# Performance work log

Hardware: AMD Instinct MI355X
Metric: run time of the kernel (lower is better)

## Reference

```python
import jax, jax.numpy as jnp
import numpy as np

V, E, H, S, B = 32000, 512, 512, 512, 32  # vocab, emb=n_unit, hidden, srclen, batch


def _lstm_zero_state_step(x, W_ih, b_ih, b_hh):
    """PyTorch LSTM single step with zero initial (h, c).
    With h0 = 0, the recurrent term h0 @ W_hh^T vanishes, so W_hh does not
    affect the output (faithful to the original, which never passes state).
    Gate order i, f, g, o. Works on [..., in_dim] batched inputs.
    """
    gates = x @ W_ih.T + b_ih + b_hh
    i, f, g, o = jnp.split(gates, 4, axis=-1)
    c = jax.nn.sigmoid(i) * jnp.tanh(g)  # f gate multiplies c0 = 0
    h = jax.nn.sigmoid(o) * jnp.tanh(c)
    return h, c


def setup_inputs() -> dict:
    key = jax.random.key(0)
    ks = jax.random.split(key, 10)
    s = 1.0 / np.sqrt(H)
    return {
        "src_seqs": jax.random.randint(ks[0], (S, B), 0, V),
        "W_emb": jax.random.normal(ks[1], (V, E), dtype=jnp.float32) * 0.02,
        # read LSTM (E -> H)
        "W_ih_r": jax.random.uniform(ks[2], (4 * H, E), minval=-s, maxval=s),
        "b_ih_r": jax.random.uniform(ks[3], (4 * H,), minval=-s, maxval=s),
        "b_hh_r": jax.random.uniform(ks[4], (4 * H,), minval=-s, maxval=s),
        # compose MLP (2H -> 2H)
        "W_c": jax.random.uniform(ks[5], (2 * H, 2 * H), minval=-s, maxval=s),
        "b_c": jax.random.uniform(ks[6], (2 * H,), minval=-s, maxval=s),
        # write LSTM (2H -> H)
        "W_ih_w": jax.random.uniform(ks[7], (4 * H, 2 * H), minval=-s, maxval=s),
        "b_ih_w": jax.random.uniform(ks[8], (4 * H,), minval=-s, maxval=s),
        "b_hh_w": jax.random.uniform(ks[9], (4 * H,), minval=-s, maxval=s),
    }


def reference(src_seqs, W_emb, W_ih_r, b_ih_r, b_hh_r, W_c, b_c,
              W_ih_w, b_ih_w, b_hh_w):
    emb = W_emb[src_seqs]                     # [S, B, E]
    # read LSTM is stateless per step (zero init state each call) -> vectorize
    o_all, _ = _lstm_zero_state_step(emb, W_ih_r, b_ih_r, b_hh_r)  # [S, B, H]
    M0 = jnp.transpose(emb, (1, 0, 2))        # [B, S, H] memory

    def step(M, o_t):
        # read: attention over memory
        z = jax.nn.softmax(jnp.einsum('bsh,bh->bs', M, o_t), axis=1)  # [B, S]
        m = jnp.einsum('bs,bsh->bh', z, M)                            # [B, H]
        # compose
        c_in = jnp.concatenate([o_t, m], axis=1) @ W_c.T + b_c        # [B, 2H]
        # write LSTM (also stateless per call)
        h, cell = _lstm_zero_state_step(c_in, W_ih_w, b_ih_w, b_hh_w)  # [B, H]
        # erase/write memory update
        M_new = (1.0 - z)[..., None] * M + z[..., None] * h[:, None, :]
        return M_new, (h, cell)

    _, (hs, cells) = jax.lax.scan(step, M0, o_all)
    outputs = hs                              # [S, B, H]
    h_n = hs[-1][None]                        # [1, B, H] (n_layer=1)
    c_n = cells[-1][None]                     # [1, B, H]
    return outputs, h_n, c_n
```

## Files before the change

kernel.cpp:

```cpp
#include <hip/hip_runtime.h>
#include <hip/hip_bf16.h>

#define S_LEN 512
#define B_SZ  32
#define H_DIM 512
#define KC    1024

typedef __attribute__((ext_vector_type(8)))  short  short8;
typedef __attribute__((ext_vector_type(4)))  float  f32x4;
typedef __attribute__((ext_vector_type(2)))  float  f32x2;

static __device__ __forceinline__ unsigned short f2bf(float f){
  unsigned u = __float_as_uint(f);
  u += 0x7fffu + ((u >> 16) & 1u);
  return (unsigned short)(u >> 16);
}
static __device__ __forceinline__ short8 cvt8(float4 a, float4 b){
  short8 r;
  r[0]=(short)f2bf(a.x); r[1]=(short)f2bf(a.y); r[2]=(short)f2bf(a.z); r[3]=(short)f2bf(a.w);
  r[4]=(short)f2bf(b.x); r[5]=(short)f2bf(b.y); r[6]=(short)f2bf(b.z); r[7]=(short)f2bf(b.w);
  return r;
}
static __device__ __forceinline__ float sigf(float x){ return 1.0f/(1.0f+__expf(-x)); }
static __device__ __forceinline__ float tanh_(float x){
  float e = __expf(2.0f*x);
  return (e-1.0f)/(e+1.0f);
}

__global__ __launch_bounds__(256) void k_gather_emb(const int* __restrict__ src,
    const float* __restrict__ Wemb, unsigned short* __restrict__ embB){
  int gid = blockIdx.x*256 + threadIdx.x;
  int row = gid >> 6;
  int k   = (gid & 63) * 8;
  int idx = src[row];
  const float* p = Wemb + (size_t)idx*H_DIM + k;
  float4 a = *(const float4*)p;
  float4 b = *(const float4*)(p+4);
  *(short8*)(embB + (size_t)gid*8) = cvt8(a,b);
}

__global__ __launch_bounds__(256) void k_perm_wr(const float* __restrict__ W,
    unsigned short* __restrict__ out){
  int gid = blockIdx.x*256 + threadIdx.x;
  int n = gid >> 6;
  int k = (gid & 63)*8;
  int j = (n&3)*512 + (n>>2);
  const float* p = W + (size_t)j*512 + k;
  float4 a = *(const float4*)p;
  float4 b = *(const float4*)(p+4);
  *(short8*)(out + (size_t)gid*8) = cvt8(a,b);
}

__global__ __launch_bounds__(256) void k_perm_wihw(const float* __restrict__ W,
    unsigned short* __restrict__ out){
  int gid = blockIdx.x*256 + threadIdx.x;
  int n = gid >> 7;
  int k = (gid & 127)*8;
  int j = (n&3)*512 + (n>>2);
  const float* p = W + (size_t)j*KC + k;
  float4 a = *(const float4*)p;
  float4 b = *(const float4*)(p+4);
  *(short8*)(out + (size_t)gid*8) = cvt8(a,b);
}

__global__ __launch_bounds__(256) void k_wcT(const float* __restrict__ Wc,
    unsigned short* __restrict__ out){
  __shared__ float tile[64][65];
  int bx = blockIdx.x & 15, by = blockIdx.x >> 4;
  int c0 = bx*64, r0 = by*64;
  int row = threadIdx.x >> 2;
  int cp  = (threadIdx.x & 3)*16;
  for (int i=0;i<16;i+=4){
    float4 v = *(const float4*)&Wc[(size_t)(r0+row)*KC + c0 + cp + i];
    tile[row][cp+i+0]=v.x; tile[row][cp+i+1]=v.y; tile[row][cp+i+2]=v.z; tile[row][cp+i+3]=v.w;
  }
  __syncthreads();
  short8 s0, s1;
  for(int i=0;i<8;++i){
    s0[i]=(short)f2bf(tile[cp+i][row]);
    s1[i]=(short)f2bf(tile[cp+8+i][row]);
  }
  unsigned short* op = out + (size_t)(c0+row)*KC + r0 + cp;
  *(short8*)op = s0; *(short8*)(op+8) = s1;
}

__global__ __launch_bounds__(256) void k_bias_r(const float* __restrict__ bi,
    const float* __restrict__ bh, float* __restrict__ out){
  int n = blockIdx.x*256 + threadIdx.x;
  int j = (n&3)*512 + (n>>2);
  out[n] = bi[j] + bh[j];
}

__global__ __launch_bounds__(256) void k_bcomb(const float* __restrict__ Wihw,
    const float* __restrict__ bc, const float* __restrict__ bi,
    const float* __restrict__ bh, float* __restrict__ out){
  int n = blockIdx.x*256 + threadIdx.x;
  int j = (n&3)*512 + (n>>2);
  const float* wp = Wihw + (size_t)j*KC;
  float s = 0.f;
  for (int l=0;l<KC;l+=4){
    float4 w = *(const float4*)&wp[l];
    float4 c = *(const float4*)&bc[l];
    s += w.x*c.x + w.y*c.y + w.z*c.z + w.w*c.w;
  }
  out[n] = s + bi[j] + bh[j];
}

template<int EPI>
__global__ __launch_bounds__(256) void gemm_k(const unsigned short* __restrict__ A,
    const unsigned short* __restrict__ Bm, int K, int bStride, int bnCnt,
    const float* __restrict__ bias, float* __restrict__ outF,
    unsigned short* __restrict__ outB, short* __restrict__ outI, int outStride){
  __shared__ __align__(16) char smem[66560];
  unsigned short* As = (unsigned short*)smem;
  unsigned short* Bs = As + 128*72;
  float* epi = (float*)smem;
  const int tid = threadIdx.x, lane = tid & 63, w = tid >> 6;
  const int wr = w >> 1, wc = w & 1;
  const int bm = blockIdx.x / bnCnt, bn = blockIdx.x % bnCnt;
  f32x4 acc[4][4] = {};
  const size_t Abase = (size_t)bm*128*K;
  const size_t Bbase = (size_t)bn*128*bStride;
  for (int k0 = 0; k0 < K; k0 += 64){
    __syncthreads();
    #pragma unroll
    for (int i = 0; i < 4; ++i){
      int idx = tid + i*256;
      int row = idx >> 3, cb = (idx & 7)*8;
      *(short8*)&As[row*72 + cb] = *(const short8*)&A[Abase + (size_t)row*K + k0 + cb];
      *(short8*)&Bs[row*72 + cb] = *(const short8*)&Bm[Bbase + (size_t)row*bStride + k0 + cb];
    }
    __syncthreads();
    #pragma unroll
    for (int kk = 0; kk < 64; kk += 32){
      short8 af[4], bf[4];
      #pragma unroll
      for (int i=0;i<4;++i) af[i] = *(short8*)&As[(wr*64 + i*16 + (lane&15))*72 + kk + (lane>>4)*8];
      #pragma unroll
      for (int j=0;j<4;++j) bf[j] = *(short8*)&Bs[(wc*64 + j*16 + (lane&15))*72 + kk + (lane>>4)*8];
      #pragma unroll
      for (int i=0;i<4;++i)
        #pragma unroll
        for (int j=0;j<4;++j)
          acc[i][j] = __builtin_amdgcn_mfma_f32_16x16x32_bf16(af[i], bf[j], acc[i][j], 0,0,0);
    }
  }
  if (EPI == 0){
    float bj[4];
    #pragma unroll
    for (int j=0;j<4;++j) bj[j] = bias[bn*128 + wc*64 + j*16 + (lane&15)];
    __syncthreads();
    float* ep = epi + w*(64*65);
    #pragma unroll
    for (int i=0;i<4;++i)
      #pragma unroll
      for (int j=0;j<4;++j)
        #pragma unroll
        for (int r=0;r<4;++r)
          ep[(i*16 + (lane>>4)*4 + r)*65 + j*16 + (lane&15)] = acc[i][j][r] + bj[j];
    __syncthreads();
    int rg = bm*128 + wr*64 + lane;
    #pragma unroll
    for (int q=0;q<16;++q){
      float gi = ep[lane*65 + q*4+0];
      float gg = ep[lane*65 + q*4+2];
      float go = ep[lane*65 + q*4+3];
      float c = sigf(gi)*tanh_(gg);
      float h = sigf(go)*tanh_(c);
      int cg = bn*32 + wc*16 + q;
      outF[(size_t)rg*H_DIM + cg] = h;
      outB[(size_t)rg*H_DIM + cg] = f2bf(h);
    }
  } else if (EPI == 1){
    #pragma unroll
    for (int i=0;i<4;++i)
      #pragma unroll
      for (int j=0;j<4;++j)
        #pragma unroll
        for (int r=0;r<4;++r){
          int rg = bm*128 + wr*64 + i*16 + (lane>>4)*4 + r;
          int cg = bn*128 + wc*64 + j*16 + (lane&15);
          outB[(size_t)rg*outStride + cg] = f2bf(acc[i][j][r]);
        }
  } else {
    #pragma unroll
    for (int i=0;i<4;++i)
      #pragma unroll
      for (int j=0;j<4;++j)
        #pragma unroll
        for (int r=0;r<4;++r){
          int rg = bm*128 + wr*64 + i*16 + (lane>>4)*4 + r;
          int cg = bn*128 + wc*64 + j*16 + (lane&15);
          float v = acc[i][j][r] * 4096.0f;
          v = fminf(fmaxf(v, -32767.0f), 32767.0f);
          outI[(size_t)rg*outStride + cg] = (short)__float2int_rn(v);
        }
  }
}

__global__ __launch_bounds__(256,1) void scan_k(
    const int* __restrict__ src, const float* __restrict__ Wemb,
    const float* __restrict__ o_all, const unsigned short* __restrict__ Wcomb,
    const float* __restrict__ bcomb, const short* __restrict__ gatesO,
    float* __restrict__ dpart, float* __restrict__ gpart,
    float* __restrict__ out, int* __restrict__ cnts){
  __shared__ __align__(16) float M[512*66];
  __shared__ __align__(16) float ubuf[2048];
  __shared__ float z_lds[512];
  __shared__ float o_lds[64];
  __shared__ float h_lds[64];
  __shared__ float m_lds[64];
  __shared__ float gg[256];
  __shared__ float red4[4];

  const int tid = threadIdx.x, lane = tid & 63, wv = tid >> 6;
  const int bid = blockIdx.x;
  const int c = bid & 7, b = bid >> 3;
  int* dcnt = cnts + b*64;
  int* gcnt = cnts + 2048 + b*64;
  float* dslot = dpart + ((size_t)b*8 + c)*512;
  float* gslot = gpart + ((size_t)b*8 + c)*2048;

  short8 wf[64];
  {
    const unsigned short* wbase = Wcomb + 512 + c*64 + (lane>>4)*8;
    #pragma unroll
    for (int i=0;i<32;++i){
      int n = (wv*32 + i)*16 + (lane&15);
      const unsigned short* wp = wbase + (size_t)n*KC;
      wf[i*2+0] = *(const short8*)(wp);
      wf[i*2+1] = *(const short8*)(wp + 32);
    }
  }

  if (tid < 64){ h_lds[tid] = 0.f; }
  z_lds[tid] = 0.f; z_lds[tid+256] = 0.f;
  #pragma unroll
  for (int r=0;r<2;++r){
    int s = tid + r*256;
    int idx = src[s*B_SZ + b];
    const float* wp = Wemb + (size_t)idx*H_DIM + c*64;
    float* mp = &M[s*66];
    #pragma unroll
    for (int k=0;k<64;k+=4){
      float4 v = *(const float4*)&wp[k];
      *(f32x2*)&mp[k]   = (f32x2){v.x, v.y};
      *(f32x2*)&mp[k+2] = (f32x2){v.z, v.w};
    }
  }
  float o_pref = 0.f;
  if (tid < 64) o_pref = o_all[(size_t)b*H_DIM + c*64 + tid];
  float gO_pref = (float)gatesO[(size_t)b*2048 + c*256 + tid] * (1.0f/4096.0f);
  __syncthreads();

  for (int t=0; t<S_LEN; ++t){
    if (tid < 64) o_lds[tid] = o_pref;
    float gO = gO_pref;
    __syncthreads();

    #pragma unroll
    for (int r=0;r<2;++r){
      int s = tid + r*256;
      float zp = z_lds[s];
      float* mp = &M[s*66];
      float dd = 0.f;
      #pragma unroll
      for (int k=0;k<64;k+=2){
        f32x2 v = *(f32x2*)&mp[k];
        f32x2 h2 = *(f32x2*)&h_lds[k];
        f32x2 o2 = *(f32x2*)&o_lds[k];
        v[0] += zp*(h2[0]-v[0]); v[1] += zp*(h2[1]-v[1]);
        *(f32x2*)&mp[k] = v;
        dd += v[0]*o2[0] + v[1]*o2[1];
      }
      ubuf[s] = dd;
    }
    __syncthreads();
    {
      f32x2 v = *(f32x2*)&ubuf[2*tid];
      float* p = dslot + 2*tid;
      asm volatile("global_store_dwordx2 %0, %1, off sc0 sc1" :: "v"(p), "v"(v) : "memory");
    }

    asm volatile("s_waitcnt vmcnt(0)" ::: "memory");
    if (tid == 0){
      __hip_atomic_fetch_add(dcnt, 1, __ATOMIC_RELAXED, __HIP_MEMORY_SCOPE_AGENT);
      int tg = 8*(t+1);
      while (__hip_atomic_load(dcnt, __ATOMIC_RELAXED, __HIP_MEMORY_SCOPE_AGENT) < tg)
        __builtin_amdgcn_s_sleep(1);
    }
    __syncthreads();
    asm volatile("" ::: "memory");

    float d0, d1;
    {
      const float* p0 = dpart + (size_t)b*8*512 + 2*tid;
      f32x2 a0,a1,a2,a3,a4,a5,a6,a7;
      asm volatile(
        "global_load_dwordx2 %0, %8, off sc0 sc1\n\t"
        "global_load_dwordx2 %1, %9, off sc0 sc1\n\t"
        "global_load_dwordx2 %2, %10, off sc0 sc1\n\t"
        "global_load_dwordx2 %3, %11, off sc0 sc1\n\t"
        "global_load_dwordx2 %4, %12, off sc0 sc1\n\t"
        "global_load_dwordx2 %5, %13, off sc0 sc1\n\t"
        "global_load_dwordx2 %6, %14, off sc0 sc1\n\t"
        "global_load_dwordx2 %7, %15, off sc0 sc1\n\t"
        "s_waitcnt vmcnt(0)"
        : "=&v"(a0),"=&v"(a1),"=&v"(a2),"=&v"(a3),
          "=&v"(a4),"=&v"(a5),"=&v"(a6),"=&v"(a7)
        : "v"(p0), "v"(p0+512), "v"(p0+1024), "v"(p0+1536),
          "v"(p0+2048), "v"(p0+2560), "v"(p0+3072), "v"(p0+3584)
        : "memory");
      d0 = ((a0[0]+a1[0])+(a2[0]+a3[0])) + ((a4[0]+a5[0])+(a6[0]+a7[0]));
      d1 = ((a0[1]+a1[1])+(a2[1]+a3[1])) + ((a4[1]+a5[1])+(a6[1]+a7[1]));
    }
    float mx, sm;
    {
      float v = fmaxf(d0, d1);
      #pragma unroll
      for (int m2=32;m2>0;m2>>=1) v = fmaxf(v, __shfl_xor(v, m2));
      __syncthreads();
      if (lane==0) red4[wv] = v;
      __syncthreads();
      mx = fmaxf(fmaxf(red4[0],red4[1]), fmaxf(red4[2],red4[3]));
    }
    float ex0 = __expf(d0 - mx), ex1 = __expf(d1 - mx);
    {
      float v = ex0 + ex1;
      #pragma unroll
      for (int m2=32;m2>0;m2>>=1) v += __shfl_xor(v, m2);
      __syncthreads();
      if (lane==0) red4[wv] = v;
      __syncthreads();
      sm = (red4[0]+red4[1]) + (red4[2]+red4[3]);
    }
    float inv = 1.f / sm;
    z_lds[2*tid]   = ex0*inv;
    z_lds[2*tid+1] = ex1*inv;
    {
      int tn = (t < S_LEN-1) ? t+1 : t;
      if (tid < 64) o_pref = o_all[((size_t)tn*B_SZ + b)*H_DIM + c*64 + tid];
      gO_pref = (float)gatesO[((size_t)tn*B_SZ + b)*2048 + c*256 + tid] * (1.0f/4096.0f);
    }
    __syncthreads();

    {
      float* part4 = ubuf;
      int col = tid & 63;
      int s0 = wv*128;
      float mp = 0.f;
      #pragma unroll 8
      for (int s2=0;s2<128;++s2)
        mp += z_lds[s0+s2]*M[(s0+s2)*66 + col];
      part4[wv*64 + col] = mp;
    }
    __syncthreads();
    if (tid < 64)
      m_lds[tid] = (ubuf[tid]+ubuf[64+tid]) + (ubuf[128+tid]+ubuf[192+tid]);
    __syncthreads();

    {
      short8 a0 = {0,0,0,0,0,0,0,0}, a1 = a0;
      if ((lane & 15) == 0){
        int kq = (lane>>4)*8;
        #pragma unroll
        for (int j=0;j<8;++j){
          a0[j] = (short)f2bf(m_lds[kq+j]);
          a1[j] = (short)f2bf(m_lds[32+kq+j]);
        }
      }
      float* gstage = ubuf;
      #pragma unroll
      for (int i=0;i<32;++i){
        f32x4 acc = {0.f,0.f,0.f,0.f};
        acc = __builtin_amdgcn_mfma_f32_16x16x32_bf16(a0, wf[i*2+0], acc, 0,0,0);
        acc = __builtin_amdgcn_mfma_f32_16x16x32_bf16(a1, wf[i*2+1], acc, 0,0,0);
        if (lane < 16) gstage[wv*512 + i*16 + lane] = acc[0];
      }
    }
    __syncthreads();
    {
      f32x4 g0 = *(f32x4*)&ubuf[8*tid];
      f32x4 g1 = *(f32x4*)&ubuf[8*tid+4];
      float* p = gslot + 8*tid;
      asm volatile(
        "global_store_dwordx4 %0, %2, off sc0 sc1\n\t"
        "global_store_dwordx4 %1, %3, off sc0 sc1"
        :: "v"(p), "v"(p+4), "v"(g0), "v"(g1) : "memory");
    }

    asm volatile("s_waitcnt vmcnt(0)" ::: "memory");
    if (tid == 0){
      __hip_atomic_fetch_add(gcnt, 1, __ATOMIC_RELAXED, __HIP_MEMORY_SCOPE_AGENT);
      int tg = 8*(t+1);
      while (__hip_atomic_load(gcnt, __ATOMIC_RELAXED, __HIP_MEMORY_SCOPE_AGENT) < tg)
        __builtin_amdgcn_s_sleep(1);
    }
    __syncthreads();
    asm volatile("" ::: "memory");

    {
      const float* gp = gpart + ((size_t)b*8 + (tid>>5))*2048 + c*256 + (tid&31)*8;
      f32x4 f0, f1;
      asm volatile(
        "global_load_dwordx4 %0, %2, off sc0 sc1\n\t"
        "global_load_dwordx4 %1, %3, off sc0 sc1\n\t"
        "s_waitcnt vmcnt(0)"
        : "=&v"(f0), "=&v"(f1)
        : "v"(gp), "v"(gp+4) : "memory");
      float* gsum = ubuf;
      *(f32x4*)&gsum[(tid>>5)*256 + (tid&31)*8]     = f0;
      *(f32x4*)&gsum[(tid>>5)*256 + (tid&31)*8 + 4] = f1;
    }
    __syncthreads();
    {
      float gv = gO + bcomb[c*256 + tid];
      #pragma unroll
      for (int c2=0;c2<8;++c2) gv += ubuf[c2*256 + tid];
      gg[tid] = gv;
    }
    __syncthreads();
    if (tid < 64){
      float gi = gg[tid*4+0];
      float gG = gg[tid*4+2];
      float go = gg[tid*4+3];
      float ccv = sigf(gi)*tanh_(gG);
      float hh  = sigf(go)*tanh_(ccv);
      h_lds[tid] = hh;
      int hq = c*64 + tid;
      out[((size_t)t*B_SZ + b)*H_DIM + hq] = hh;
      if (t == S_LEN-1){
        out[(size_t)S_LEN*B_SZ*H_DIM + (size_t)b*H_DIM + hq] = hh;
        out[(size_t)S_LEN*B_SZ*H_DIM + (size_t)B_SZ*H_DIM + (size_t)b*H_DIM + hq] = ccv;
      }
    }
    __syncthreads();
  }
}

extern "C" void kernel_launch(void* const* d_in, const int* in_sizes, int n_in,
                              void* d_out, int out_size, void* d_ws, size_t ws_size,
                              hipStream_t stream){
  const int*   src   = (const int*)  d_in[0];
  const float* Wemb  = (const float*)d_in[1];
  const float* Wihr  = (const float*)d_in[2];
  const float* bihr  = (const float*)d_in[3];
  const float* bhhr  = (const float*)d_in[4];
  const float* Wc    = (const float*)d_in[5];
  const float* bc    = (const float*)d_in[6];
  const float* Wihw  = (const float*)d_in[7];
  const float* bihw  = (const float*)d_in[8];
  const float* bhhw  = (const float*)d_in[9];
  float* out = (float*)d_out;

  char* ws = (char*)d_ws;
  size_t off = 0;
  auto alloc = [&](size_t bytes)->char*{
    char* p = ws + off; off += (bytes + 255) & ~(size_t)255; return p;
  };
  unsigned short* embB  = (unsigned short*)alloc((size_t)16384*512*2);
  float*          o_all = (float*)         alloc((size_t)16384*512*4);
  unsigned short* o_allB= (unsigned short*)alloc((size_t)16384*512*2);
  unsigned short* WrP   = (unsigned short*)alloc((size_t)2048*512*2);
  unsigned short* WiwP  = (unsigned short*)alloc((size_t)2048*1024*2);
  unsigned short* WcT   = (unsigned short*)alloc((size_t)1024*1024*2);
  unsigned short* Wcomb = (unsigned short*)alloc((size_t)2048*1024*2);
  float*          bperm = (float*)alloc(2048*4);
  float*          bcomb = (float*)alloc(2048*4);
  short*          gatesO= (short*)alloc((size_t)16384*2048*2);
  float*          dpart = (float*)alloc((size_t)32*8*512*4);
  float*          gpart = (float*)alloc((size_t)32*8*2048*4);
  int*            cnts  = (int*)  alloc(16384);

  hipMemsetAsync(cnts, 0, 16384, stream);
  k_gather_emb<<<4096,256,0,stream>>>(src, Wemb, embB);
  k_perm_wr  <<<512, 256,0,stream>>>(Wihr, WrP);
  k_perm_wihw<<<1024,256,0,stream>>>(Wihw, WiwP);
  k_wcT      <<<256, 256,0,stream>>>(Wc, WcT);
  k_bias_r   <<<8,   256,0,stream>>>(bihr, bhhr, bperm);
  k_bcomb    <<<8,   256,0,stream>>>(Wihw, bc, bihw, bhhw, bcomb);
  gemm_k<0><<<2048,256,0,stream>>>(embB, WrP, 512, 512, 16, bperm, o_all, o_allB, nullptr, H_DIM);
  gemm_k<1><<<128,256,0,stream>>>(WiwP, WcT, 1024, 1024, 8, nullptr, nullptr, Wcomb, nullptr, 1024);
  gemm_k<2><<<2048,256,0,stream>>>(o_allB, Wcomb, 512, 1024, 16, nullptr, nullptr, nullptr, gatesO, 2048);
  scan_k<<<256,256,0,stream>>>(src, Wemb, o_all, Wcomb, bcomb, gatesO,
                               dpart, gpart, out, cnts);
}
```

Baseline: 6.177 ms.

## Exchange attention vector m across blocks instead of partial gate sums

```diff
diff --git a/kernel.cpp b/kernel.cpp
--- a/kernel.cpp
+++ b/kernel.cpp
@@ -202,89 +202,76 @@
     const int* __restrict__ src, const float* __restrict__ Wemb,
     const float* __restrict__ o_all, const unsigned short* __restrict__ Wcomb,
     const float* __restrict__ bcomb, const short* __restrict__ gatesO,
-    float* __restrict__ dpart, float* __restrict__ gpart,
+    float* __restrict__ dpart, float* __restrict__ mpart,
     float* __restrict__ out, int* __restrict__ cnts){
   __shared__ __align__(16) float M[512*66];
-  __shared__ __align__(16) float ubuf[2048];
-  __shared__ float z_lds[512];
-  __shared__ float o_lds[64];
+  __shared__ __align__(16) float dstage[512];
+  __shared__ __align__(16) float m_full[512];
+  __shared__ __align__(16) float z_lds[512];
+  __shared__ float part4[256];
+  __shared__ float gsum[256];
+  __shared__ float m_sl[64];
+  __shared__ float o_sl[64];
   __shared__ float h_lds[64];
-  __shared__ float m_lds[64];
-  __shared__ float gg[256];
   __shared__ float red4[4];
 
   const int tid = threadIdx.x, lane = tid & 63, wv = tid >> 6;
   const int bid = blockIdx.x;
   const int c = bid & 7, b = bid >> 3;
+  const int r15 = lane & 15, kq = lane >> 4;
   int* dcnt = cnts + b*64;
-  int* gcnt = cnts + 2048 + b*64;
+  int* mcnt = cnts + 2048 + b*64;
   float* dslot = dpart + ((size_t)b*8 + c)*512;
-  float* gslot = gpart + ((size_t)b*8 + c)*2048;
+  float* mslot = mpart + (size_t)b*512 + c*64;
 
   short8 wf[64];
-  {
-    const unsigned short* wbase = Wcomb + 512 + c*64 + (lane>>4)*8;
-    #pragma unroll
-    for (int i=0;i<32;++i){
-      int n = (wv*32 + i)*16 + (lane&15);
-      const unsigned short* wp = wbase + (size_t)n*KC;
-      wf[i*2+0] = *(const short8*)(wp);
-      wf[i*2+1] = *(const short8*)(wp + 32);
-    }
-  }
-
-  if (tid < 64){ h_lds[tid] = 0.f; }
+  #pragma unroll
+  for (int ct=0; ct<4; ++ct)
+    #pragma unroll
+    for (int kf=0; kf<16; ++kf)
+      wf[ct*16+kf] = *(const short8*)&Wcomb[
+        (size_t)(c*256 + wv*64 + ct*16 + r15)*KC + 512 + kf*32 + kq*8];
+
   z_lds[tid] = 0.f; z_lds[tid+256] = 0.f;
+  if (tid < 64){
+    h_lds[tid] = 0.f;
+    o_sl[tid] = o_all[(size_t)b*H_DIM + c*64 + tid];
+  }
+  __syncthreads();
   #pragma unroll
   for (int r=0;r<2;++r){
     int s = tid + r*256;
     int idx = src[s*B_SZ + b];
     const float* wp = Wemb + (size_t)idx*H_DIM + c*64;
     float* mp = &M[s*66];
+    float dd = 0.f;
     #pragma unroll
     for (int k=0;k<64;k+=4){
       float4 v = *(const float4*)&wp[k];
       *(f32x2*)&mp[k]   = (f32x2){v.x, v.y};
       *(f32x2*)&mp[k+2] = (f32x2){v.z, v.w};
-    }
-  }
-  float o_pref = 0.f;
-  if (tid < 64) o_pref = o_all[(size_t)b*H_DIM + c*64 + tid];
-  float gO_pref = (float)gatesO[(size_t)b*2048 + c*256 + tid] * (1.0f/4096.0f);
+      dd += v.x*o_sl[k] + v.y*o_sl[k+1] + v.z*o_sl[k+2] + v.w*o_sl[k+3];
+    }
+    dstage[s] = dd;
+  }
   __syncthreads();
+  {
+    f32x2 v = *(f32x2*)&dstage[2*tid];
+    float* p = dslot + 2*tid;
+    asm volatile("global_store_dwordx2 %0, %1, off sc0 sc1" :: "v"(p), "v"(v) : "memory");
+  }
+  asm volatile("s_waitcnt vmcnt(0)" ::: "memory");
+  __syncthreads();
+  if (tid == 0)
+    __hip_atomic_fetch_add(dcnt, 1, __ATOMIC_RELAXED, __HIP_MEMORY_SCOPE_AGENT);
 
   for (int t=0; t<S_LEN; ++t){
-    if (tid < 64) o_lds[tid] = o_pref;
-    float gO = gO_pref;
-    __syncthreads();
-
-    #pragma unroll
-    for (int r=0;r<2;++r){
-      int s = tid + r*256;
-      float zp = z_lds[s];
-      float* mp = &M[s*66];
-      float dd = 0.f;
-      #pragma unroll
-      for (int k=0;k<64;k+=2){
-        f32x2 v = *(f32x2*)&mp[k];
-        f32x2 h2 = *(f32x2*)&h_lds[k];
-        f32x2 o2 = *(f32x2*)&o_lds[k];
-        v[0] += zp*(h2[0]-v[0]); v[1] += zp*(h2[1]-v[1]);
-        *(f32x2*)&mp[k] = v;
-        dd += v[0]*o2[0] + v[1]*o2[1];
-      }
-      ubuf[s] = dd;
-    }
-    __syncthreads();
-    {
-      f32x2 v = *(f32x2*)&ubuf[2*tid];
-      float* p = dslot + 2*tid;
-      asm volatile("global_store_dwordx2 %0, %1, off sc0 sc1" :: "v"(p), "v"(v) : "memory");
-    }
-
-    asm volatile("s_waitcnt vmcnt(0)" ::: "memory");
+    const int tn = (t < S_LEN-1) ? t+1 : t;
+    float opf = 0.f;
+    if (tid < 64) opf = o_all[((size_t)tn*B_SZ + b)*H_DIM + c*64 + tid];
+    float gO = (float)gatesO[((size_t)t*B_SZ + b)*2048 + c*256 + tid] * (1.0f/4096.0f);
+
     if (tid == 0){
-      __hip_atomic_fetch_add(dcnt, 1, __ATOMIC_RELAXED, __HIP_MEMORY_SCOPE_AGENT);
       int tg = 8*(t+1);
       while (__hip_atomic_load(dcnt, __ATOMIC_RELAXED, __HIP_MEMORY_SCOPE_AGENT) < tg)
         __builtin_amdgcn_s_sleep(1);
@@ -337,15 +324,9 @@
     float inv = 1.f / sm;
     z_lds[2*tid]   = ex0*inv;
     z_lds[2*tid+1] = ex1*inv;
-    {
-      int tn = (t < S_LEN-1) ? t+1 : t;
-      if (tid < 64) o_pref = o_all[((size_t)tn*B_SZ + b)*H_DIM + c*64 + tid];
-      gO_pref = (float)gatesO[((size_t)tn*B_SZ + b)*2048 + c*256 + tid] * (1.0f/4096.0f);
-    }
-    __syncthreads();
-
-    {
-      float* part4 = ubuf;
+    __syncthreads();
+
+    {
       int col = tid & 63;
       int s0 = wv*128;
       float mp = 0.f;
@@ -356,74 +337,73 @@
     }
     __syncthreads();
     if (tid < 64)
-      m_lds[tid] = (ubuf[tid]+ubuf[64+tid]) + (ubuf[128+tid]+ubuf[192+tid]);
-    __syncthreads();
-
-    {
-      short8 a0 = {0,0,0,0,0,0,0,0}, a1 = a0;
-      if ((lane & 15) == 0){
-        int kq = (lane>>4)*8;
-        #pragma unroll
-        for (int j=0;j<8;++j){
-          a0[j] = (short)f2bf(m_lds[kq+j]);
-          a1[j] = (short)f2bf(m_lds[32+kq+j]);
+      m_sl[tid] = (part4[tid]+part4[64+tid]) + (part4[128+tid]+part4[192+tid]);
+    __syncthreads();
+    if (tid < 16){
+      f32x4 v = *(f32x4*)&m_sl[tid*4];
+      float* p = mslot + tid*4;
+      asm volatile("global_store_dwordx4 %0, %1, off sc0 sc1" :: "v"(p), "v"(v) : "memory");
+    }
+    asm volatile("s_waitcnt vmcnt(0)" ::: "memory");
+    __syncthreads();
+    if (tid == 0){
+      __hip_atomic_fetch_add(mcnt, 1, __ATOMIC_RELAXED, __HIP_MEMORY_SCOPE_AGENT);
+      int tg = 8*(t+1);
+      while (__hip_atomic_load(mcnt, __ATOMIC_RELAXED, __HIP_MEMORY_SCOPE_AGENT) < tg)
+        __builtin_amdgcn_s_sleep(1);
+    }
+    __syncthreads();
+    asm volatile("" ::: "memory");
+
+    {
+      const float* p = mpart + (size_t)b*512 + 2*tid;
+      f32x2 v;
+      asm volatile(
+        "global_load_dwordx2 %0, %1, off sc0 sc1\n\t"
+        "s_waitcnt vmcnt(0)" : "=&v"(v) : "v"(p) : "memory");
+      m_full[2*tid] = v[0]; m_full[2*tid+1] = v[1];
+    }
+    __syncthreads();
+
+    {
+      short8 a[16];
+      #pragma unroll
+      for (int kf=0; kf<16; ++kf){
+        short8 v = {0,0,0,0,0,0,0,0};
+        if (r15 == 0){
+          int kb = kf*32 + kq*8;
+          #pragma unroll
+          for (int j=0;j<8;++j) v[j] = (short)f2bf(m_full[kb+j]);
         }
-      }
-      float* gstage = ubuf;
-      #pragma unroll
-      for (int i=0;i<32;++i){
-        f32x4 acc = {0.f,0.f,0.f,0.f};
-        acc = __builtin_amdgcn_mfma_f32_16x16x32_bf16(a0, wf[i*2+0], acc, 0,0,0);
-        acc = __builtin_amdgcn_mfma_f32_16x16x32_bf16(a1, wf[i*2+1], acc, 0,0,0);
-        if (lane < 16) gstage[wv*512 + i*16 + lane] = acc[0];
-      }
-    }
-    __syncthreads();
-    {
-      f32x4 g0 = *(f32x4*)&ubuf[8*tid];
-      f32x4 g1 = *(f32x4*)&ubuf[8*tid+4];
-      float* p = gslot + 8*tid;
-      asm volatile(
-        "global_store_dwordx4 %0, %2, off sc0 sc1\n\t"
-        "global_store_dwordx4 %1, %3, off sc0 sc1"
-        :: "v"(p), "v"(p+4), "v"(g0), "v"(g1) : "memory");
-    }
-
-    asm volatile("s_waitcnt vmcnt(0)" ::: "memory");
-    if (tid == 0){
-      __hip_atomic_fetch_add(gcnt, 1, __ATOMIC_RELAXED, __HIP_MEMORY_SCOPE_AGENT);
-      int tg = 8*(t+1);
-      while (__hip_atomic_load(gcnt, __ATOMIC_RELAXED, __HIP_MEMORY_SCOPE_AGENT) < tg)
-        __builtin_amdgcn_s_sleep(1);
-    }
-    __syncthreads();
-    asm volatile("" ::: "memory");
-
-    {
-      const float* gp = gpart + ((size_t)b*8 + (tid>>5))*2048 + c*256 + (tid&31)*8;
-      f32x4 f0, f1;
-      asm volatile(
-        "global_load_dwordx4 %0, %2, off sc0 sc1\n\t"
-        "global_load_dwordx4 %1, %3, off sc0 sc1\n\t"
-        "s_waitcnt vmcnt(0)"
-        : "=&v"(f0), "=&v"(f1)
-        : "v"(gp), "v"(gp+4) : "memory");
-      float* gsum = ubuf;
-      *(f32x4*)&gsum[(tid>>5)*256 + (tid&31)*8]     = f0;
-      *(f32x4*)&gsum[(tid>>5)*256 + (tid&31)*8 + 4] = f1;
-    }
-    __syncthreads();
-    {
-      float gv = gO + bcomb[c*256 + tid];
-      #pragma unroll
-      for (int c2=0;c2<8;++c2) gv += ubuf[c2*256 + tid];
-      gg[tid] = gv;
+        a[kf] = v;
+      }
+      f32x4 acc0 = {0,0,0,0}, acc1 = acc0, acc2 = acc0, acc3 = acc0;
+      #pragma unroll
+      for (int kf=0; kf<16; ++kf){
+        acc0 = __builtin_amdgcn_mfma_f32_16x16x32_bf16(a[kf], wf[kf],    acc0, 0,0,0);
+        acc1 = __builtin_amdgcn_mfma_f32_16x16x32_bf16(a[kf], wf[16+kf], acc1, 0,0,0);
+        acc2 = __builtin_amdgcn_mfma_f32_16x16x32_bf16(a[kf], wf[32+kf], acc2, 0,0,0);
+        acc3 = __builtin_amdgcn_mfma_f32_16x16x32_bf16(a[kf], wf[48+kf], acc3, 0,0,0);
+      }
+      if (lane < 16){
+        gsum[wv*64 + lane]      = acc0[0];
+        gsum[wv*64 + 16 + lane] = acc1[0];
+        gsum[wv*64 + 32 + lane] = acc2[0];
+        gsum[wv*64 + 48 + lane] = acc3[0];
+      }
+    }
+    __syncthreads();
+
+    {
+      float gv = gsum[tid] + gO + bcomb[c*256 + tid];
+      __syncthreads();
+      part4[tid] = gv;
     }
     __syncthreads();
     if (tid < 64){
-      float gi = gg[tid*4+0];
-      float gG = gg[tid*4+2];
-      float go = gg[tid*4+3];
+      float gi = part4[tid*4+0];
+      float gG = part4[tid*4+2];
+      float go = part4[tid*4+3];
       float ccv = sigf(gi)*tanh_(gG);
       float hh  = sigf(go)*tanh_(ccv);
       h_lds[tid] = hh;
@@ -433,8 +413,39 @@
         out[(size_t)S_LEN*B_SZ*H_DIM + (size_t)b*H_DIM + hq] = hh;
         out[(size_t)S_LEN*B_SZ*H_DIM + (size_t)B_SZ*H_DIM + (size_t)b*H_DIM + hq] = ccv;
       }
-    }
-    __syncthreads();
+      o_sl[tid] = opf;
+    }
+    __syncthreads();
+
+    if (t < S_LEN-1){
+      #pragma unroll
+      for (int r=0;r<2;++r){
+        int s = tid + r*256;
+        float zp = z_lds[s];
+        float* mp = &M[s*66];
+        float dd = 0.f;
+        #pragma unroll
+        for (int k=0;k<64;k+=2){
+          f32x2 v = *(f32x2*)&mp[k];
+          f32x2 h2 = *(f32x2*)&h_lds[k];
+          f32x2 o2 = *(f32x2*)&o_sl[k];
+          v[0] += zp*(h2[0]-v[0]); v[1] += zp*(h2[1]-v[1]);
+          *(f32x2*)&mp[k] = v;
+          dd += v[0]*o2[0] + v[1]*o2[1];
+        }
+        dstage[s] = dd;
+      }
+      __syncthreads();
+      {
+        f32x2 v = *(f32x2*)&dstage[2*tid];
+        float* p = dslot + 2*tid;
+        asm volatile("global_store_dwordx2 %0, %1, off sc0 sc1" :: "v"(p), "v"(v) : "memory");
+      }
+      asm volatile("s_waitcnt vmcnt(0)" ::: "memory");
+      __syncthreads();
+      if (tid == 0)
+        __hip_atomic_fetch_add(dcnt, 1, __ATOMIC_RELAXED, __HIP_MEMORY_SCOPE_AGENT);
+    }
   }
 }
 
@@ -469,7 +480,7 @@
   float*          bcomb = (float*)alloc(2048*4);
   short*          gatesO= (short*)alloc((size_t)16384*2048*2);
   float*          dpart = (float*)alloc((size_t)32*8*512*4);
-  float*          gpart = (float*)alloc((size_t)32*8*2048*4);
+  float*          mpart = (float*)alloc((size_t)32*512*4);
   int*            cnts  = (int*)  alloc(16384);
 
   hipMemsetAsync(cnts, 0, 16384, stream);
@@ -483,5 +494,5 @@
   gemm_k<1><<<128,256,0,stream>>>(WiwP, WcT, 1024, 1024, 8, nullptr, nullptr, Wcomb, nullptr, 1024);
   gemm_k<2><<<2048,256,0,stream>>>(o_allB, Wcomb, 512, 1024, 16, nullptr, nullptr, nullptr, gatesO, 2048);
   scan_k<<<256,256,0,stream>>>(src, Wemb, o_all, Wcomb, bcomb, gatesO,
-                               dpart, gpart, out, cnts);
-}
+                               dpart, mpart, out, cnts);
+}
```

New measurement: 6.410 ms. 3.8% more time.
